# Kernel optimization log

Hardware: AMD Instinct MI355X
Metric: run time of the kernel (lower is better)

## Reference

```python
import jax, jax.numpy as jnp
from jax import lax
import numpy as np

T, B, DIN, NQ = 256, 2048, 128, 16  # hidden_dim == n_qubits (required by module math)


def setup_inputs() -> dict:
    key = jax.random.key(0)
    k1, k2, k3 = jax.random.split(key, 3)
    inputs = jax.random.normal(k1, (T, B, DIN), dtype=jnp.float32)
    # stacked params for the 4 gates: forget, input, update, output
    W = jax.random.normal(k2, (4, NQ, DIN + NQ), dtype=jnp.float32) * 0.1
    b = jnp.zeros((4, NQ), dtype=jnp.float32)
    theta = jax.random.normal(k3, (4, NQ), dtype=jnp.float32)
    return {"inputs": inputs, "W": W, "b": b, "theta": theta}


def reference(inputs, W, b, theta):
    # Analytic simulation of each QGate circuit:
    #   RX(x_i) then RX(theta_i) on wire i  ->  product state, <Z_i> = cos(x_i + theta_i)
    #   CNOT chain (0->1, 1->2, ...): Heisenberg picture maps Z_k -> Z_0 Z_1 ... Z_k,
    Tn, Bn, _ = inputs.shape
    nq = theta.shape[-1]
    h0 = jnp.zeros((Bn, nq), dtype=inputs.dtype)
    c0 = jnp.zeros((Bn, nq), dtype=inputs.dtype)

    def step(carry, x):
        hx, cx = carry
        combined = jnp.concatenate([x, hx], axis=1)              # [B, Din+H]
        z = jnp.einsum('bd,gnd->bgn', combined, W) + b           # [B, 4, nq]
        q = jnp.cumprod(jnp.cos(z + theta), axis=-1)             # quantum gate expectations
        f = jax.nn.sigmoid(q[:, 0])
        i = jax.nn.sigmoid(q[:, 1])
        g = jnp.tanh(q[:, 2])
        o = jax.nn.sigmoid(q[:, 3])
        cx = f * cx + i * g
        hx = o * jnp.tanh(cx)
        return (hx, cx), hx

    (hx, cx), outputs = lax.scan(step, (h0, c0), inputs)
    return outputs, hx, cx
```

## Files before the change

kernel.cpp:

```cpp
#include <hip/hip_runtime.h>
#include <hip/hip_bf16.h>
#include <stdint.h>


#define T_STEPS 256
#define BATCH   2048
#define DIN     128
#define NQ      16
#define LCOLS   64
#define DTOT    144
#define NTILE   16
#define ZROW    68

typedef __attribute__((ext_vector_type(8))) short bf16x8;
typedef __attribute__((ext_vector_type(4))) float f32x4;
typedef __attribute__((ext_vector_type(2))) int   int2v;

#if defined(__has_builtin)
#if __has_builtin(__builtin_amdgcn_permlane16_swap) && __has_builtin(__builtin_amdgcn_permlane32_swap)
#define USE_PLSWAP 1
#endif
#endif
#ifndef USE_PLSWAP
#define USE_PLSWAP 0
#endif

__device__ __forceinline__ float bf2f(unsigned short u) {
    union { unsigned int i; float f; } v; v.i = ((unsigned int)u) << 16; return v.f;
}
__device__ __forceinline__ unsigned short f2bf(float f) {
    union { float f; unsigned int i; } v; v.f = f;
    unsigned int i = v.i;
    unsigned int r = i + 0x7fffu + ((i >> 16) & 1u);
    return (unsigned short)(r >> 16);
}
__device__ __forceinline__ float ldval(const float* p) { return *p; }
__device__ __forceinline__ float ldval(const unsigned short* p) { return bf2f(*p); }

__device__ __forceinline__ int detect_bf16(const unsigned int* __restrict__ xw, int lane) {
    int cnt = 0;
#pragma unroll
    for (int i = 0; i < 4; ++i) {
        unsigned int w = xw[lane + i * 64];
        unsigned int e = (w >> 7) & 0xFFu;
        cnt += (e >= 100u && e <= 140u) ? 1 : 0;
    }
#pragma unroll
    for (int d = 32; d > 0; d >>= 1) cnt += __shfl_down(cnt, d, 64);
    int tot = __shfl(cnt, 0, 64);
    return (tot >= 140) ? 1 : 0;
}

template <int CTRL>
__device__ __forceinline__ float dpp_sh(float v) {
    int r = __builtin_amdgcn_update_dpp(__builtin_bit_cast(int, 1.0f),
                                        __builtin_bit_cast(int, v),
                                        CTRL, 0xF, 0xF, false);
    return __builtin_bit_cast(float, r);
}
template <int CTRL>
__device__ __forceinline__ float rot16(float v) {
    int r = __builtin_amdgcn_update_dpp(0, __builtin_bit_cast(int, v),
                                        CTRL, 0xF, 0xF, false);
    return __builtin_bit_cast(float, r);
}

template <int BASE>
__device__ __forceinline__ void qstep(int t, int g, int n, float cur,
                                      const float (&Wp)[16], float& h, float& c,
                                      float& hsave, float* __restrict__ out, int b,
                                      bool m0, bool m1,
                                      int a_f, int a_i, int a_g, int a_o)
{
    float h1  = rot16<0x121>(h), h2  = rot16<0x122>(h), h3  = rot16<0x123>(h);
    float h4  = rot16<0x124>(h), h5  = rot16<0x125>(h), h6  = rot16<0x126>(h), h7  = rot16<0x127>(h);
    float h8  = rot16<0x128>(h), h9  = rot16<0x129>(h), h10 = rot16<0x12A>(h), h11 = rot16<0x12B>(h);
    float h12 = rot16<0x12C>(h), h13 = rot16<0x12D>(h), h14 = rot16<0x12E>(h), h15 = rot16<0x12F>(h);

    float s0 = fmaf(Wp[0],  h,   fmaf(Wp[1],  h1,  fmaf(Wp[2],  h2,  Wp[3]  * h3)));
    float s1 = fmaf(Wp[4],  h4,  fmaf(Wp[5],  h5,  fmaf(Wp[6],  h6,  Wp[7]  * h7)));
    float s2 = fmaf(Wp[8],  h8,  fmaf(Wp[9],  h9,  fmaf(Wp[10], h10, Wp[11] * h11)));
    float s3 = fmaf(Wp[12], h12, fmaf(Wp[13], h13, fmaf(Wp[14], h14, Wp[15] * h15)));
    float z = cur + ((s0 + s1) + (s2 + s3));

    float cz = __cosf(z);
    cz *= dpp_sh<BASE + 1>(cz);
    cz *= dpp_sh<BASE + 2>(cz);
    cz *= dpp_sh<BASE + 4>(cz);
    cz *= dpp_sh<BASE + 8>(cz);

    float a = (g == 2) ? 2.f * cz : cz;
    float e = __expf(-a);
    float rr = __builtin_amdgcn_rcpf(1.f + e);
    float s = (g == 2) ? (1.f - e) * rr : rr;

    float fv, iv, gv, ov;
#if USE_PLSWAP
    int si = __builtin_bit_cast(int, s);
    int2v e1 = __builtin_amdgcn_permlane16_swap(si, si, false, false);
    int c1i = m0 ? e1[0] : e1[1];
    int2v e2 = __builtin_amdgcn_permlane32_swap(si, si, false, false);
    int c2i = m1 ? e2[0] : e2[1];
    int2v e3 = __builtin_amdgcn_permlane16_swap(c2i, c2i, false, false);
    int c3i = m0 ? e3[0] : e3[1];
    float C0 = s;
    float C1 = __builtin_bit_cast(float, c1i);
    float C2 = __builtin_bit_cast(float, c2i);
    float C3 = __builtin_bit_cast(float, c3i);
    float P  = m1 ? C2 : C0;
    float Q  = m1 ? C3 : C1;
    float R_ = m1 ? C0 : C2;
    float S_ = m1 ? C1 : C3;
    fv = m0 ? Q  : P;
    iv = m0 ? P  : Q;
    gv = m0 ? S_ : R_;
    ov = m0 ? R_ : S_;
#else
    int si = __builtin_bit_cast(int, s);
    fv = __builtin_bit_cast(float, __builtin_amdgcn_ds_bpermute(a_f, si));
    iv = __builtin_bit_cast(float, __builtin_amdgcn_ds_bpermute(a_i, si));
    gv = __builtin_bit_cast(float, __builtin_amdgcn_ds_bpermute(a_g, si));
    ov = __builtin_bit_cast(float, __builtin_amdgcn_ds_bpermute(a_o, si));
#endif

    c = fmaf(fv, c, iv * gv);
    float e2t = __expf(-2.f * c);
    float tc = (1.f - e2t) * __builtin_amdgcn_rcpf(1.f + e2t);
    h = ov * tc;

    if ((t & 3) == g) hsave = h;
    if ((t & 3) == 3)
        out[(size_t)(t - 3 + g) * (BATCH * NQ) + (size_t)b * NQ + n] = hsave;
}

template <int BASE, typename InT>
__device__ __forceinline__ void fused_main(
    const InT* __restrict__ x, const InT* __restrict__ W,
    const InT* __restrict__ bv, const InT* __restrict__ th,
    float* __restrict__ out, int b, int lane,
    const float (&Wp)[16], float (*zt)[16][ZROW])
{
    const int m = lane & 15, quad = lane >> 4;
    const int g = quad, n = m;
    const bool m0 = (g & 1) != 0, m1 = (g & 2) != 0;
    const int a_f = n << 2, a_i = (16 + n) << 2, a_g = (32 + n) << 2, a_o = (48 + n) << 2;

    bf16x8 bh[4][4], bl[4][4];
    if constexpr (sizeof(InT) == 2) {
#pragma unroll
        for (int kt = 0; kt < 4; ++kt)
#pragma unroll
            for (int nb = 0; nb < 4; ++nb)
                bh[kt][nb] = *(const bf16x8*)((const unsigned short*)W +
                             (size_t)(nb * 16 + m) * DTOT + kt * 32 + quad * 8);
    } else {
#pragma unroll
        for (int kt = 0; kt < 4; ++kt)
#pragma unroll
            for (int nb = 0; nb < 4; ++nb) {
                const float* p = (const float*)W + (size_t)(nb * 16 + m) * DTOT + kt * 32 + quad * 8;
#pragma unroll
                for (int j = 0; j < 8; ++j) {
                    float wv = p[j];
                    unsigned short hh = f2bf(wv);
                    bh[kt][nb][j] = (short)hh;
                    bl[kt][nb][j] = (short)f2bf(wv - bf2f(hh));
                }
            }
    }
    const float bias = ldval(bv + lane) + ldval(th + lane);

    const InT* xbase = x + ((size_t)m * BATCH + (size_t)b) * DIN + quad * 8;

    f32x4 rx[8]; bf16x8 rbx[4];
    auto LOAD = [&](int tl) {
        const InT* p = xbase + (size_t)tl * ((size_t)16 * BATCH * DIN);
#pragma unroll
        for (int kt = 0; kt < 4; ++kt) {
            if constexpr (sizeof(InT) == 2) {
                rbx[kt] = *(const bf16x8*)(p + kt * 32);
            } else {
                rx[2 * kt]     = *(const f32x4*)((const float*)p + kt * 32);
                rx[2 * kt + 1] = *(const f32x4*)((const float*)p + kt * 32 + 4);
            }
        }
    };
    auto PRODUCE = [&](int tl) {
        f32x4 acc[4] = {};
#pragma unroll
        for (int kt = 0; kt < 4; ++kt) {
            if constexpr (sizeof(InT) == 2) {
#pragma unroll
                for (int nb = 0; nb < 4; ++nb)
                    acc[nb] = __builtin_amdgcn_mfma_f32_16x16x32_bf16(rbx[kt], bh[kt][nb], acc[nb], 0, 0, 0);
            } else {
                bf16x8 ah, al;
#pragma unroll
                for (int j = 0; j < 8; ++j) {
                    float xv = rx[2 * kt + (j >> 2)][j & 3];
                    unsigned short hh = f2bf(xv);
                    ah[j] = (short)hh;
                    al[j] = (short)f2bf(xv - bf2f(hh));
                }
#pragma unroll
                for (int nb = 0; nb < 4; ++nb)
                    acc[nb] = __builtin_amdgcn_mfma_f32_16x16x32_bf16(ah, bh[kt][nb], acc[nb], 0, 0, 0);
#pragma unroll
                for (int nb = 0; nb < 4; ++nb)
                    acc[nb] = __builtin_amdgcn_mfma_f32_16x16x32_bf16(al, bh[kt][nb], acc[nb], 0, 0, 0);
#pragma unroll
                for (int nb = 0; nb < 4; ++nb)
                    acc[nb] = __builtin_amdgcn_mfma_f32_16x16x32_bf16(ah, bl[kt][nb], acc[nb], 0, 0, 0);
            }
        }
        const int buf = tl & 1;
#pragma unroll
        for (int nb = 0; nb < 4; ++nb)
#pragma unroll
            for (int r = 0; r < 4; ++r)
                zt[buf][quad * 4 + r][nb * 16 + m] = acc[nb][r];
    };

    float h = 0.f, c = 0.f, hsave = 0.f;

    LOAD(0);
    PRODUCE(0);
    LOAD(1);

#pragma unroll 1
    for (int tl = 0; tl < NTILE; ++tl) {
        const int buf = tl & 1;
        const int t0 = tl * 16;
        float zr0[8], zr1[8];
#pragma unroll
        for (int j = 0; j < 8; ++j) zr0[j] = zt[buf][j][lane] + bias;
        if (tl < NTILE - 1) PRODUCE(tl + 1);
        if (tl < NTILE - 2) LOAD(tl + 2);
#pragma unroll
        for (int j = 0; j < 4; ++j)
            qstep<BASE>(t0 + j, g, n, zr0[j], Wp, h, c, hsave, out, b, m0, m1, a_f, a_i, a_g, a_o);
#pragma unroll
        for (int j = 0; j < 8; ++j) zr1[j] = zt[buf][8 + j][lane] + bias;
#pragma unroll
        for (int j = 4; j < 8; ++j)
            qstep<BASE>(t0 + j, g, n, zr0[j], Wp, h, c, hsave, out, b, m0, m1, a_f, a_i, a_g, a_o);
#pragma unroll
        for (int j = 0; j < 8; ++j)
            qstep<BASE>(t0 + 8 + j, g, n, zr1[j], Wp, h, c, hsave, out, b, m0, m1, a_f, a_i, a_g, a_o);
    }

    if (g == 0) {
        out[(size_t)T_STEPS * BATCH * NQ + (size_t)b * NQ + n] = h;
        out[(size_t)T_STEPS * BATCH * NQ + (size_t)BATCH * NQ + (size_t)b * NQ + n] = c;
    }
}

__global__ __launch_bounds__(256, 2) void qlstm_fused(
    const void* __restrict__ x_, const void* __restrict__ W_,
    const void* __restrict__ b_, const void* __restrict__ th_,
    float* __restrict__ out)
{
    __shared__ float zw[4][2][16][ZROW];

    const int lane = threadIdx.x & 63;
    const int w    = threadIdx.x >> 6;
    const int b    = blockIdx.x * 4 + w;
    const int n    = lane & 15;

    const int isbf = __builtin_amdgcn_readfirstlane(detect_bf16((const unsigned int*)x_, lane));

    int pr  = __builtin_amdgcn_update_dpp(0, lane, 0x121, 0xF, 0xF, false);
    int p0r = __shfl(pr, 0, 64);
    const int d = (p0r == 1) ? 1 : 15;

    float Wp[16];
    if (isbf) {
        const unsigned short* W = (const unsigned short*)W_;
#pragma unroll
        for (int k = 0; k < 16; ++k)
            Wp[k] = bf2f(W[(size_t)lane * DTOT + DIN + ((n + k * d) & 15)]);
    } else {
        const float* W = (const float*)W_;
#pragma unroll
        for (int k = 0; k < 16; ++k)
            Wp[k] = W[(size_t)lane * DTOT + DIN + ((n + k * d) & 15)];
    }

    int probe = __builtin_amdgcn_update_dpp(999, lane, 0x111, 0xF, 0xF, false);
    int p2 = __shfl(probe, 2, 64);

    if (isbf) {
        if (p2 == 1) fused_main<0x110, unsigned short>((const unsigned short*)x_, (const unsigned short*)W_,
                                                       (const unsigned short*)b_, (const unsigned short*)th_,
                                                       out, b, lane, Wp, zw[w]);
        else         fused_main<0x100, unsigned short>((const unsigned short*)x_, (const unsigned short*)W_,
                                                       (const unsigned short*)b_, (const unsigned short*)th_,
                                                       out, b, lane, Wp, zw[w]);
    } else {
        if (p2 == 1) fused_main<0x110, float>((const float*)x_, (const float*)W_,
                                              (const float*)b_, (const float*)th_,
                                              out, b, lane, Wp, zw[w]);
        else         fused_main<0x100, float>((const float*)x_, (const float*)W_,
                                              (const float*)b_, (const float*)th_,
                                              out, b, lane, Wp, zw[w]);
    }
}

extern "C" void kernel_launch(void* const* d_in, const int* in_sizes, int n_in,
                              void* d_out, int out_size, void* d_ws, size_t ws_size,
                              hipStream_t stream) {
    const void* x  = d_in[0];
    const void* W  = d_in[1];
    const void* bv = d_in[2];
    const void* th = d_in[3];
    (void)d_ws; (void)ws_size;
    qlstm_fused<<<BATCH / 4, 256, 0, stream>>>(x, W, bv, th, (float*)d_out);
}
```

Before: 407.5 us.

## Move W fragments to shared LDS and single-buffer the z tile

```diff
diff --git a/kernel.cpp b/kernel.cpp
--- a/kernel.cpp
+++ b/kernel.cpp
@@ -7,10 +7,9 @@
 #define BATCH   2048
 #define DIN     128
 #define NQ      16
-#define LCOLS   64
 #define DTOT    144
 #define NTILE   16
-#define ZROW    68
+#define ZROW    66
 
 typedef __attribute__((ext_vector_type(8))) short bf16x8;
 typedef __attribute__((ext_vector_type(4))) float f32x4;
@@ -137,38 +136,38 @@
 __device__ __forceinline__ void fused_main(
     const InT* __restrict__ x, const InT* __restrict__ W,
     const InT* __restrict__ bv, const InT* __restrict__ th,
-    float* __restrict__ out, int b, int lane,
-    const float (&Wp)[16], float (*zt)[16][ZROW])
+    float* __restrict__ out, int b, int w, int lane,
+    const float (&Wp)[16], float (*zt)[ZROW],
+    bf16x8 (*wfh)[64], bf16x8 (*wfl)[64])
 {
     const int m = lane & 15, quad = lane >> 4;
     const int g = quad, n = m;
     const bool m0 = (g & 1) != 0, m1 = (g & 2) != 0;
     const int a_f = n << 2, a_i = (16 + n) << 2, a_g = (32 + n) << 2, a_o = (48 + n) << 2;
 
-    bf16x8 bh[4][4], bl[4][4];
     if constexpr (sizeof(InT) == 2) {
 #pragma unroll
-        for (int kt = 0; kt < 4; ++kt)
-#pragma unroll
-            for (int nb = 0; nb < 4; ++nb)
-                bh[kt][nb] = *(const bf16x8*)((const unsigned short*)W +
-                             (size_t)(nb * 16 + m) * DTOT + kt * 32 + quad * 8);
+        for (int nb = 0; nb < 4; ++nb)
+            wfh[w * 4 + nb][lane] = *(const bf16x8*)((const unsigned short*)W +
+                                    (size_t)(nb * 16 + m) * DTOT + w * 32 + quad * 8);
     } else {
 #pragma unroll
-        for (int kt = 0; kt < 4; ++kt)
-#pragma unroll
-            for (int nb = 0; nb < 4; ++nb) {
-                const float* p = (const float*)W + (size_t)(nb * 16 + m) * DTOT + kt * 32 + quad * 8;
-#pragma unroll
-                for (int j = 0; j < 8; ++j) {
-                    float wv = p[j];
-                    unsigned short hh = f2bf(wv);
-                    bh[kt][nb][j] = (short)hh;
-                    bl[kt][nb][j] = (short)f2bf(wv - bf2f(hh));
-                }
+        for (int nb = 0; nb < 4; ++nb) {
+            const float* p = (const float*)W + (size_t)(nb * 16 + m) * DTOT + w * 32 + quad * 8;
+            bf16x8 ah, al;
+#pragma unroll
+            for (int j = 0; j < 8; ++j) {
+                float wv = p[j];
+                unsigned short hh = f2bf(wv);
+                ah[j] = (short)hh;
+                al[j] = (short)f2bf(wv - bf2f(hh));
             }
+            wfh[w * 4 + nb][lane] = ah;
+            wfl[w * 4 + nb][lane] = al;
+        }
     }
     const float bias = ldval(bv + lane) + ldval(th + lane);
+    __syncthreads();
 
     const InT* xbase = x + ((size_t)m * BATCH + (size_t)b) * DIN + quad * 8;
 
@@ -185,14 +184,14 @@
             }
         }
     };
-    auto PRODUCE = [&](int tl) {
+    auto PRODUCE = [&]() {
         f32x4 acc[4] = {};
 #pragma unroll
         for (int kt = 0; kt < 4; ++kt) {
             if constexpr (sizeof(InT) == 2) {
 #pragma unroll
                 for (int nb = 0; nb < 4; ++nb)
-                    acc[nb] = __builtin_amdgcn_mfma_f32_16x16x32_bf16(rbx[kt], bh[kt][nb], acc[nb], 0, 0, 0);
+                    acc[nb] = __builtin_amdgcn_mfma_f32_16x16x32_bf16(rbx[kt], wfh[kt * 4 + nb][lane], acc[nb], 0, 0, 0);
             } else {
                 bf16x8 ah, al;
 #pragma unroll
@@ -204,49 +203,39 @@
                 }
 #pragma unroll
                 for (int nb = 0; nb < 4; ++nb)
-                    acc[nb] = __builtin_amdgcn_mfma_f32_16x16x32_bf16(ah, bh[kt][nb], acc[nb], 0, 0, 0);
+                    acc[nb] = __builtin_amdgcn_mfma_f32_16x16x32_bf16(ah, wfh[kt * 4 + nb][lane], acc[nb], 0, 0, 0);
 #pragma unroll
                 for (int nb = 0; nb < 4; ++nb)
-                    acc[nb] = __builtin_amdgcn_mfma_f32_16x16x32_bf16(al, bh[kt][nb], acc[nb], 0, 0, 0);
+                    acc[nb] = __builtin_amdgcn_mfma_f32_16x16x32_bf16(al, wfh[kt * 4 + nb][lane], acc[nb], 0, 0, 0);
 #pragma unroll
                 for (int nb = 0; nb < 4; ++nb)
-                    acc[nb] = __builtin_amdgcn_mfma_f32_16x16x32_bf16(ah, bl[kt][nb], acc[nb], 0, 0, 0);
+                    acc[nb] = __builtin_amdgcn_mfma_f32_16x16x32_bf16(ah, wfl[kt * 4 + nb][lane], acc[nb], 0, 0, 0);
             }
         }
-        const int buf = tl & 1;
 #pragma unroll
         for (int nb = 0; nb < 4; ++nb)
 #pragma unroll
             for (int r = 0; r < 4; ++r)
-                zt[buf][quad * 4 + r][nb * 16 + m] = acc[nb][r];
+                zt[quad * 4 + r][nb * 16 + m] = acc[nb][r];
     };
 
     float h = 0.f, c = 0.f, hsave = 0.f;
 
     LOAD(0);
-    PRODUCE(0);
+    PRODUCE();
     LOAD(1);
 
 #pragma unroll 1
     for (int tl = 0; tl < NTILE; ++tl) {
-        const int buf = tl & 1;
         const int t0 = tl * 16;
-        float zr0[8], zr1[8];
-#pragma unroll
-        for (int j = 0; j < 8; ++j) zr0[j] = zt[buf][j][lane] + bias;
-        if (tl < NTILE - 1) PRODUCE(tl + 1);
+        float zr[16];
+#pragma unroll
+        for (int j = 0; j < 16; ++j) zr[j] = zt[j][lane] + bias;
+        if (tl < NTILE - 1) PRODUCE();
         if (tl < NTILE - 2) LOAD(tl + 2);
 #pragma unroll
-        for (int j = 0; j < 4; ++j)
-            qstep<BASE>(t0 + j, g, n, zr0[j], Wp, h, c, hsave, out, b, m0, m1, a_f, a_i, a_g, a_o);
-#pragma unroll
-        for (int j = 0; j < 8; ++j) zr1[j] = zt[buf][8 + j][lane] + bias;
-#pragma unroll
-        for (int j = 4; j < 8; ++j)
-            qstep<BASE>(t0 + j, g, n, zr0[j], Wp, h, c, hsave, out, b, m0, m1, a_f, a_i, a_g, a_o);
-#pragma unroll
-        for (int j = 0; j < 8; ++j)
-            qstep<BASE>(t0 + 8 + j, g, n, zr1[j], Wp, h, c, hsave, out, b, m0, m1, a_f, a_i, a_g, a_o);
+        for (int j = 0; j < 16; ++j)
+            qstep<BASE>(t0 + j, g, n, zr[j], Wp, h, c, hsave, out, b, m0, m1, a_f, a_i, a_g, a_o);
     }
 
     if (g == 0) {
@@ -260,7 +249,9 @@
     const void* __restrict__ b_, const void* __restrict__ th_,
     float* __restrict__ out)
 {
-    __shared__ float zw[4][2][16][ZROW];
+    __shared__ float  zw[4][NTILE][ZROW];
+    __shared__ bf16x8 wfh[16][64];
+    __shared__ bf16x8 wfl[16][64];
 
     const int lane = threadIdx.x & 63;
     const int w    = threadIdx.x >> 6;
@@ -292,17 +283,17 @@
     if (isbf) {
         if (p2 == 1) fused_main<0x110, unsigned short>((const unsigned short*)x_, (const unsigned short*)W_,
                                                        (const unsigned short*)b_, (const unsigned short*)th_,
-                                                       out, b, lane, Wp, zw[w]);
+                                                       out, b, w, lane, Wp, zw[w], wfh, wfl);
         else         fused_main<0x100, unsigned short>((const unsigned short*)x_, (const unsigned short*)W_,
                                                        (const unsigned short*)b_, (const unsigned short*)th_,
-                                                       out, b, lane, Wp, zw[w]);
+                                                       out, b, w, lane, Wp, zw[w], wfh, wfl);
     } else {
         if (p2 == 1) fused_main<0x110, float>((const float*)x_, (const float*)W_,
                                               (const float*)b_, (const float*)th_,
-                                              out, b, lane, Wp, zw[w]);
+                                              out, b, w, lane, Wp, zw[w], wfh, wfl);
         else         fused_main<0x100, float>((const float*)x_, (const float*)W_,
                                               (const float*)b_, (const float*)th_,
-                                              out, b, lane, Wp, zw[w]);
+                                              out, b, w, lane, Wp, zw[w], wfh, wfl);
     }
 }
 
```

Measured after the change: 401.4 us. Within noise of the previous version (-1.5%).
